# Kernel tuning notes

Hardware: AMD Instinct MI355X
Metric: run time of the kernel (lower is better)

The kernel has to match this reference:

```python
import jax, jax.numpy as jnp
import numpy as np

B, T = 64, 2048
QD, KD, VD, AD = 512, 512, 512, 256


def setup_inputs() -> dict:
    key = jax.random.key(0)
    ks = jax.random.split(key, 9)
    s = lambda d: 1.0 / np.sqrt(d)
    return {
        "query": jax.random.normal(ks[0], (B, QD), jnp.float32),
        "key": jax.random.normal(ks[1], (B, T, KD), jnp.float32),
        "value": jax.random.normal(ks[2], (B, T, VD), jnp.float32),
        "Wq": jax.random.uniform(ks[3], (QD, AD), jnp.float32, -s(QD), s(QD)),
        "bq": jax.random.uniform(ks[4], (AD,), jnp.float32, -s(QD), s(QD)),
        "Wk": jax.random.uniform(ks[5], (KD, AD), jnp.float32, -s(KD), s(KD)),
        "bk": jax.random.uniform(ks[6], (AD,), jnp.float32, -s(KD), s(KD)),
        "Wo": jax.random.uniform(ks[7], (AD, 1), jnp.float32, -s(AD), s(AD)),
        "bo": jax.random.uniform(ks[8], (1,), jnp.float32, -s(AD), s(AD)),
    }


def reference(query, key, value, Wq, bq, Wk, bk, Wo, bo):
    # q_proj: [B, 1, AD]; k_proj: [B, T, AD]
    q_proj = (query @ Wq + bq)[:, None, :]
    k_proj = jnp.einsum("btk,ka->bta", key, Wk) + bk
    # score: [B, T, 1]
    score = jnp.tanh(q_proj + k_proj) @ Wo + bo
    attn = jax.nn.softmax(score, axis=1)  # softmax over keys (dim 1)
    # context: [B, VD] = sum_t attn[b,t] * value[b,t,:]
    context = jnp.einsum("bt,btv->bv", attn[..., 0], value)
    return context, attn[..., 0]
```

## Files before the change

kernel.cpp:

```cpp
#include <hip/hip_runtime.h>

#define NB 64
#define NT 2048
#define NQD 512
#define NKD 512
#define NVD 512
#define NAD 256

typedef __attribute__((ext_vector_type(8))) short s16x8;
typedef __attribute__((ext_vector_type(4))) float fx4;

__device__ __forceinline__ short f2bf(float x) {
  union { float f; unsigned u; } v; v.f = x;
  return (short)((v.u + 0x7fffu + ((v.u >> 16) & 1u)) >> 16);
}

__device__ __forceinline__ float fast_tanh(float x) {
  float e = __expf(x + x);
  return 1.0f - 2.0f * __builtin_amdgcn_rcpf(e + 1.0f);
}

__global__ void prep_kernel(const float* __restrict__ query, const float* __restrict__ Wq,
                            const float* __restrict__ bq, const float* __restrict__ bk,
                            const float* __restrict__ Wk,
                            float* __restrict__ qpk, short* __restrict__ WkT) {
  __shared__ float sm[64][65];
  const int tid = threadIdx.x;
  if (blockIdx.x < NB) {
    const int b = blockIdx.x;
    float* q = &sm[0][0];
    for (int k = tid; k < NQD; k += 256) q[k] = query[b * NQD + k];
    __syncthreads();
    float acc = bq[tid] + bk[tid];
#pragma unroll 8
    for (int k = 0; k < NQD; ++k) acc += q[k] * Wq[k * NAD + tid];
    qpk[b * NAD + tid] = acc;
  } else {
    const int blk = blockIdx.x - NB;
    const int kb = (blk & 7) * 64, ab = (blk >> 3) * 64;
    const int c = tid & 63, r0 = tid >> 6;
#pragma unroll
    for (int rr = r0; rr < 64; rr += 4)
      sm[rr][c] = Wk[(size_t)(kb + rr) * NAD + ab + c];
    __syncthreads();
#pragma unroll
    for (int rr = r0; rr < 64; rr += 4)
      WkT[(size_t)(ab + rr) * NKD + kb + c] = f2bf(sm[c][rr]);
  }
}

__global__ void __launch_bounds__(256, 3)
score_kernel(const float* __restrict__ key, const short* __restrict__ WkT,
             const float* __restrict__ qpk, const float* __restrict__ Wo,
             float* __restrict__ score) {
  __shared__ short As[2][4 * 64 * 8];
  __shared__ float sred[4][64];
  const int tid = threadIdx.x;
  const int w = tid >> 6, l = tid & 63;
  const int g = l >> 4, h = l & 15;
  const int m0 = blockIdx.x * 64;
  const int b = m0 >> 11;

  float qv[4], wv[4];
  const short* bp[4];
#pragma unroll
  for (int nt = 0; nt < 4; ++nt) {
    const int n = w * 64 + nt * 16 + h;
    qv[nt] = qpk[b * NAD + n];
    wv[nt] = Wo[n];
    bp[nt] = WkT + (size_t)n * NKD + g * 8;
  }

  fx4 acc[4][4];
#pragma unroll
  for (int i = 0; i < 4; ++i)
#pragma unroll
    for (int j = 0; j < 4; ++j) acc[i][j] = fx4{0.f, 0.f, 0.f, 0.f};

  const int srow = tid >> 2, sg = tid & 3;
  const float* asrc = key + (size_t)(m0 + srow) * NKD + sg * 8;
  const int sidx = ((sg * 64 + srow) * 8) ^ (sg << 3);

  s16x8 bcur[4];
  {
    fx4 a0 = *(const fx4*)asrc;
    fx4 a1 = *(const fx4*)(asrc + 4);
    s16x8 v;
    v[0]=f2bf(a0[0]); v[1]=f2bf(a0[1]); v[2]=f2bf(a0[2]); v[3]=f2bf(a0[3]);
    v[4]=f2bf(a1[0]); v[5]=f2bf(a1[1]); v[6]=f2bf(a1[2]); v[7]=f2bf(a1[3]);
    *(s16x8*)&As[0][sidx] = v;
#pragma unroll
    for (int nt = 0; nt < 4; ++nt) bcur[nt] = *(const s16x8*)bp[nt];
  }
  __syncthreads();

  int buf = 0;
#pragma unroll 2
  for (int ks = 0; ks < 16; ++ks) {
    const bool hasNext = (ks < 15);
    fx4 a0, a1;
    s16x8 bnxt[4];
    if (hasNext) {
      const float* gp = asrc + (ks + 1) * 32;
      a0 = *(const fx4*)gp;
      a1 = *(const fx4*)(gp + 4);
#pragma unroll
      for (int nt = 0; nt < 4; ++nt)
        bnxt[nt] = *(const s16x8*)(bp[nt] + (ks + 1) * 32);
    }
    s16x8 af[4];
#pragma unroll
    for (int mt = 0; mt < 4; ++mt)
      af[mt] = *(const s16x8*)&As[buf][((g * 64 + mt * 16 + h) * 8) ^ (g << 3)];
#pragma unroll
    for (int mt = 0; mt < 4; ++mt)
#pragma unroll
      for (int nt = 0; nt < 4; ++nt)
        acc[mt][nt] = __builtin_amdgcn_mfma_f32_16x16x32_bf16(af[mt], bcur[nt], acc[mt][nt], 0, 0, 0);
    if (hasNext) {
      s16x8 v;
      v[0]=f2bf(a0[0]); v[1]=f2bf(a0[1]); v[2]=f2bf(a0[2]); v[3]=f2bf(a0[3]);
      v[4]=f2bf(a1[0]); v[5]=f2bf(a1[1]); v[6]=f2bf(a1[2]); v[7]=f2bf(a1[3]);
      *(s16x8*)&As[buf ^ 1][sidx] = v;
#pragma unroll
      for (int nt = 0; nt < 4; ++nt) bcur[nt] = bnxt[nt];
    }
    __syncthreads();
    buf ^= 1;
  }

#pragma unroll
  for (int mt = 0; mt < 4; ++mt) {
#pragma unroll
    for (int r = 0; r < 4; ++r) {
      float s = fast_tanh(acc[mt][0][r] + qv[0]) * wv[0]
              + fast_tanh(acc[mt][1][r] + qv[1]) * wv[1]
              + fast_tanh(acc[mt][2][r] + qv[2]) * wv[2]
              + fast_tanh(acc[mt][3][r] + qv[3]) * wv[3];
#pragma unroll
      for (int off = 1; off < 16; off <<= 1) s += __shfl_xor(s, off, 64);
      if (h == 0) sred[w][mt * 16 + g * 4 + r] = s;
    }
  }
  __syncthreads();
  if (tid < 64)
    score[m0 + tid] = sred[0][tid] + sred[1][tid] + sred[2][tid] + sred[3][tid];
}

__global__ void softmax_kernel(const float* __restrict__ score, float* __restrict__ attn) {
  __shared__ float redm[4];
  __shared__ float reds[4];
  const int b = blockIdx.x, tid = threadIdx.x;
  const float* s = score + (size_t)b * NT;
  float v[8];
  float m = -3.0e38f;
#pragma unroll
  for (int j = 0; j < 8; ++j) { v[j] = s[tid + j * 256]; m = fmaxf(m, v[j]); }
#pragma unroll
  for (int off = 1; off < 64; off <<= 1) m = fmaxf(m, __shfl_xor(m, off, 64));
  if ((tid & 63) == 0) redm[tid >> 6] = m;
  __syncthreads();
  m = fmaxf(fmaxf(redm[0], redm[1]), fmaxf(redm[2], redm[3]));
  float sum = 0.f;
#pragma unroll
  for (int j = 0; j < 8; ++j) { v[j] = __expf(v[j] - m); sum += v[j]; }
#pragma unroll
  for (int off = 1; off < 64; off <<= 1) sum += __shfl_xor(sum, off, 64);
  if ((tid & 63) == 0) reds[tid >> 6] = sum;
  __syncthreads();
  sum = reds[0] + reds[1] + reds[2] + reds[3];
  const float inv = 1.0f / sum;
#pragma unroll
  for (int j = 0; j < 8; ++j) attn[(size_t)b * NT + tid + j * 256] = v[j] * inv;
}

__global__ void ctx_partial_kernel(const float* __restrict__ attn, const float* __restrict__ value,
                                   float* __restrict__ partial) {
  __shared__ float a[64];
  __shared__ fx4 red[128];
  const int blk = blockIdx.x;
  const int b = blk >> 5, tc = blk & 31;
  const int tid = threadIdx.x;
  if (tid < 64) a[tid] = attn[(size_t)b * NT + tc * 64 + tid];
  __syncthreads();
  const int half = tid >> 7;
  const int vi = (tid & 127) * 4;
  const float* vp = value + ((size_t)b * NT + tc * 64 + half) * NVD + vi;
  fx4 s = fx4{0.f, 0.f, 0.f, 0.f};
#pragma unroll 8
  for (int t = 0; t < 64; t += 2) {
    fx4 x = *(const fx4*)(vp + (size_t)t * NVD);
    const float wt = a[t + half];
    s += x * wt;
  }
  if (half) red[tid & 127] = s;
  __syncthreads();
  if (!half) {
    s += red[tid];
    *(fx4*)(partial + (size_t)blk * NVD + vi) = s;
  }
}

__global__ void ctx_reduce_kernel(const float* __restrict__ partial, float* __restrict__ ctx) {
  const int i = blockIdx.x * 256 + threadIdx.x;
  const int b = i >> 9, v = i & (NVD - 1);
  float s = 0.f;
#pragma unroll
  for (int tc = 0; tc < 32; ++tc) s += partial[(size_t)(b * 32 + tc) * NVD + v];
  ctx[i] = s;
}

extern "C" void kernel_launch(void* const* d_in, const int* in_sizes, int n_in,
                              void* d_out, int out_size, void* d_ws, size_t ws_size,
                              hipStream_t stream) {
  const float* query = (const float*)d_in[0];
  const float* key   = (const float*)d_in[1];
  const float* value = (const float*)d_in[2];
  const float* Wq    = (const float*)d_in[3];
  const float* bq    = (const float*)d_in[4];
  const float* Wk    = (const float*)d_in[5];
  const float* bk    = (const float*)d_in[6];
  const float* Wo    = (const float*)d_in[7];

  float* out  = (float*)d_out;
  float* ctx  = out;
  float* attn = out + NB * NVD;

  char* ws = (char*)d_ws;
  float* qpk     = (float*)(ws);
  short* WkT     = (short*)(ws + 64 * 1024);
  float* score   = (float*)(ws + (64 + 256) * 1024);
  float* partial = (float*)(ws + (64 + 256 + 512) * 1024);

  prep_kernel<<<NB + 32, 256, 0, stream>>>(query, Wq, bq, bk, Wk, qpk, WkT);
  score_kernel<<<(NB * NT) / 64, 256, 0, stream>>>(key, WkT, qpk, Wo, score);
  softmax_kernel<<<NB, 256, 0, stream>>>(score, attn);
  ctx_partial_kernel<<<NB * 32, 256, 0, stream>>>(attn, value, partial);
  ctx_reduce_kernel<<<(NB * NVD) / 256, 256, 0, stream>>>(partial, ctx);
}
```

Baseline: 186.0 us.

## Stage full bf16 key tile in LDS once and drop per-step barriers

New measurement: 194.5 us. 4.5% more time.

```diff
diff --git a/kernel.cpp b/kernel.cpp
--- a/kernel.cpp
+++ b/kernel.cpp
@@ -9,10 +9,17 @@
 
 typedef __attribute__((ext_vector_type(8))) short s16x8;
 typedef __attribute__((ext_vector_type(4))) float fx4;
+typedef __attribute__((ext_vector_type(4))) unsigned int u32x4;
 
 __device__ __forceinline__ short f2bf(float x) {
   union { float f; unsigned u; } v; v.f = x;
   return (short)((v.u + 0x7fffu + ((v.u >> 16) & 1u)) >> 16);
+}
+
+__device__ __forceinline__ unsigned cvt_pk_bf16(float lo, float hi) {
+  unsigned r;
+  asm("v_cvt_pk_bf16_f32 %0, %1, %2" : "=v"(r) : "v"(lo), "v"(hi));
+  return r;
 }
 
 __device__ __forceinline__ float fast_tanh(float x) {
@@ -49,11 +56,11 @@
   }
 }
 
-__global__ void __launch_bounds__(256, 3)
+__global__ void __launch_bounds__(256, 2)
 score_kernel(const float* __restrict__ key, const short* __restrict__ WkT,
              const float* __restrict__ qpk, const float* __restrict__ Wo,
              float* __restrict__ score) {
-  __shared__ short As[2][4 * 64 * 8];
+  __shared__ short As[64 * 512];
   __shared__ float sred[4][64];
   const int tid = threadIdx.x;
   const int w = tid >> 6, l = tid & 63;
@@ -71,39 +78,45 @@
     bp[nt] = WkT + (size_t)n * NKD + g * 8;
   }
 
+  s16x8 bcur[4];
+#pragma unroll
+  for (int nt = 0; nt < 4; ++nt) bcur[nt] = *(const s16x8*)bp[nt];
+
+  {
+    const float* tile = key + (size_t)m0 * NKD;
+#pragma unroll
+    for (int j = 0; j < 16; ++j) {
+      const int c = tid + j * 256;
+      const float* gp = tile + c * 8;
+      fx4 x0 = *(const fx4*)gp;
+      fx4 x1 = *(const fx4*)(gp + 4);
+      u32x4 pw;
+      pw[0] = cvt_pk_bf16(x0[0], x0[1]);
+      pw[1] = cvt_pk_bf16(x0[2], x0[3]);
+      pw[2] = cvt_pk_bf16(x1[0], x1[1]);
+      pw[3] = cvt_pk_bf16(x1[2], x1[3]);
+      const int row = c >> 6, col = c & 63;
+      *(u32x4*)((char*)As + ((row * 1024 + col * 16) ^ ((row & 7) << 4))) = pw;
+    }
+  }
+  __syncthreads();
+
   fx4 acc[4][4];
 #pragma unroll
   for (int i = 0; i < 4; ++i)
 #pragma unroll
     for (int j = 0; j < 4; ++j) acc[i][j] = fx4{0.f, 0.f, 0.f, 0.f};
 
-  const int srow = tid >> 2, sg = tid & 3;
-  const float* asrc = key + (size_t)(m0 + srow) * NKD + sg * 8;
-  const int sidx = ((sg * 64 + srow) * 8) ^ (sg << 3);
-
-  s16x8 bcur[4];
-  {
-    fx4 a0 = *(const fx4*)asrc;
-    fx4 a1 = *(const fx4*)(asrc + 4);
-    s16x8 v;
-    v[0]=f2bf(a0[0]); v[1]=f2bf(a0[1]); v[2]=f2bf(a0[2]); v[3]=f2bf(a0[3]);
-    v[4]=f2bf(a1[0]); v[5]=f2bf(a1[1]); v[6]=f2bf(a1[2]); v[7]=f2bf(a1[3]);
-    *(s16x8*)&As[0][sidx] = v;
-#pragma unroll
-    for (int nt = 0; nt < 4; ++nt) bcur[nt] = *(const s16x8*)bp[nt];
-  }
-  __syncthreads();
-
-  int buf = 0;
+  int abase[4];
+#pragma unroll
+  for (int mt = 0; mt < 4; ++mt) abase[mt] = (mt * 16 + h) * 1024 + g * 16;
+  const int sw = (h & 7) << 4;
+
 #pragma unroll 2
   for (int ks = 0; ks < 16; ++ks) {
     const bool hasNext = (ks < 15);
-    fx4 a0, a1;
     s16x8 bnxt[4];
     if (hasNext) {
-      const float* gp = asrc + (ks + 1) * 32;
-      a0 = *(const fx4*)gp;
-      a1 = *(const fx4*)(gp + 4);
 #pragma unroll
       for (int nt = 0; nt < 4; ++nt)
         bnxt[nt] = *(const s16x8*)(bp[nt] + (ks + 1) * 32);
@@ -111,22 +124,16 @@
     s16x8 af[4];
 #pragma unroll
     for (int mt = 0; mt < 4; ++mt)
-      af[mt] = *(const s16x8*)&As[buf][((g * 64 + mt * 16 + h) * 8) ^ (g << 3)];
+      af[mt] = *(const s16x8*)((const char*)As + ((abase[mt] + ks * 64) ^ sw));
 #pragma unroll
     for (int mt = 0; mt < 4; ++mt)
 #pragma unroll
       for (int nt = 0; nt < 4; ++nt)
         acc[mt][nt] = __builtin_amdgcn_mfma_f32_16x16x32_bf16(af[mt], bcur[nt], acc[mt][nt], 0, 0, 0);
     if (hasNext) {
-      s16x8 v;
-      v[0]=f2bf(a0[0]); v[1]=f2bf(a0[1]); v[2]=f2bf(a0[2]); v[3]=f2bf(a0[3]);
-      v[4]=f2bf(a1[0]); v[5]=f2bf(a1[1]); v[6]=f2bf(a1[2]); v[7]=f2bf(a1[3]);
-      *(s16x8*)&As[buf ^ 1][sidx] = v;
 #pragma unroll
       for (int nt = 0; nt < 4; ++nt) bcur[nt] = bnxt[nt];
     }
-    __syncthreads();
-    buf ^= 1;
   }
 
 #pragma unroll
```
